# Performance work log

Measured on AMD Instinct MI355X. Metric: run time of the kernel, lower is better.

## Reference

```python
import jax, jax.numpy as jnp
import numpy as np

D_HIDDEN = 400
D_ANCHOR = 31
N_LAYER = 24
N_HEADS = 8
DIM_HEAD = 400
D_INNER = 800
D_STATE = 16
D_CONV = 4
DT_RANK = 25  # ceil(400/16)
PE_HIDDEN = 48
EPS = 1e-5


def _point_embed(x, w, b):
    # Fourier point embedding (3DShape2VecSet PointEmbed), dim-major freq layout.
    d = x.shape[-1]
    nf = PE_HIDDEN // (2 * d)
    freqs = (2.0 ** jnp.arange(nf, dtype=x.dtype)) * jnp.pi  # [nf]
    proj = (x[..., None] * freqs).reshape(*x.shape[:-1], d * nf)  # [b,n,d*nf]
    emb = jnp.concatenate([jnp.sin(proj), jnp.cos(proj), x], axis=-1)  # [b,n,48+d]
    return emb @ w.T + b


def _rmsnorm(x, w):
    return x * jax.lax.rsqrt(jnp.mean(x * x, axis=-1, keepdims=True) + EPS) * w


def _layernorm(x, w, b):
    mu = jnp.mean(x, axis=-1, keepdims=True)
    var = jnp.var(x, axis=-1, keepdims=True)
    return (x - mu) * jax.lax.rsqrt(var + EPS) * w + b


def _selective_scan(u, dt, A, Bm, Cm, Dp):
    # u, dt: [b,l,di]; A: [di,n]; Bm, Cm: [b,l,n]; Dp: [di]
    def step(h, inp):
        u_t, dt_t, B_t, C_t = inp  # [b,di],[b,di],[b,n],[b,n]
        h = jnp.exp(dt_t[..., None] * A) * h + (dt_t * u_t)[..., None] * B_t[:, None, :]
        return h, jnp.einsum('bdn,bn->bd', h, C_t)
    h0 = jnp.zeros((u.shape[0], u.shape[2], A.shape[1]), u.dtype)
    xs = (jnp.swapaxes(u, 0, 1), jnp.swapaxes(dt, 0, 1),
          jnp.swapaxes(Bm, 0, 1), jnp.swapaxes(Cm, 0, 1))
    _, ys = jax.lax.scan(step, h0, xs)
    return jnp.swapaxes(ys, 0, 1) + u * Dp


def _mamba_block(x, norm_w, in_w, conv_w, conv_b, xproj_w, dt_w, dt_b, A_log, Dp, out_w):
    b, L, _ = x.shape
    xn = _rmsnorm(x, norm_w)
    u, z = jnp.split(xn @ in_w.T, 2, axis=-1)  # each [b,L,di]
    # causal depthwise conv1d, kernel D_CONV, left pad D_CONV-1 (torch conv truncated to L)
    u_pad = jnp.pad(u, ((0, 0), (D_CONV - 1, 0), (0, 0)))
    conv = sum(u_pad[:, k:k + L, :] * conv_w[:, k] for k in range(D_CONV)) + conv_b
    u_c = jax.nn.silu(conv)
    dbc = u_c @ xproj_w.T  # [b,L,dt_rank+2n]
    dt, Bm, Cm = jnp.split(dbc, [DT_RANK, DT_RANK + D_STATE], axis=-1)
    dt = jax.nn.softplus(dt @ dt_w.T + dt_b)  # [b,L,di]
    y = _selective_scan(u_c, dt, -jnp.exp(A_log), Bm, Cm, Dp)
    return x + (y * jax.nn.silu(z)) @ out_w.T


def _forward(mash_params, qry, anchor_w, anchor_b, point_w, point_b,
             norm_w, in_w, conv_w, conv_b, xproj_w, dt_w, dt_b, A_log, Dp, out_w,
             ln_q_w, ln_q_b, ln_c_w, ln_c_b, to_q_w, to_kv_w, to_out_w, to_out_b,
             ff_ln_w, ff_ln_b, ff_w1, ff_b1, ff_w2, ff_b2, head_w, head_b):
    # anchor embed on first 6 dims, concat remaining 25 -> [b,na,400]
    anc = _point_embed(mash_params[:, :, :6], anchor_w, anchor_b)
    x = jnp.concatenate([anc, mash_params[:, :, 6:]], axis=-1)
    for i in range(N_LAYER):
        x = _mamba_block(x, norm_w[i], in_w[i], conv_w[i], conv_b[i], xproj_w[i],
                         dt_w[i], dt_b[i], A_log[i], Dp[i], out_w[i])
    q_emb = _point_embed(qry, point_w, point_b)  # [b,nq,400]
    # PreNorm cross-attention (query norm + context norm), no residual
    qn = _layernorm(q_emb, ln_q_w, ln_q_b)
    ctx = _layernorm(x, ln_c_w, ln_c_b)
    b, nq, _ = qn.shape
    na = ctx.shape[1]
    q = (qn @ to_q_w.T).reshape(b, nq, N_HEADS, DIM_HEAD)
    k, v = jnp.split(ctx @ to_kv_w.T, 2, axis=-1)
    k = k.reshape(b, na, N_HEADS, DIM_HEAD)
    v = v.reshape(b, na, N_HEADS, DIM_HEAD)
    sim = jnp.einsum('bihd,bjhd->bhij', q, k) * (DIM_HEAD ** -0.5)
    attn = jax.nn.softmax(sim, axis=-1)
    out = jnp.einsum('bhij,bjhd->bihd', attn, v).reshape(b, nq, N_HEADS * DIM_HEAD)
    latents = out @ to_out_w.T + to_out_b  # [b,nq,400]
    # PreNorm GEGLU FeedForward with residual
    h = _layernorm(latents, ff_ln_w, ff_ln_b) @ ff_w1.T + ff_b1  # [b,nq,3200]
    a, g = jnp.split(h, 2, axis=-1)
    h = (a * jax.nn.gelu(g)) @ ff_w2.T + ff_b2
    latents = latents + h
    occ = (latents @ head_w.T + head_b).squeeze(-1)  # [b,nq]
    return occ


def setup_inputs() -> dict:
    key = jax.random.key(0)
    ks = iter(jax.random.split(key, 48))
    def nrm(shape, scale=0.02):
        return jax.random.normal(next(ks), shape, dtype=jnp.float32) * scale
    B, NA, NQ = 4, 400, 4096
    INNER = N_HEADS * DIM_HEAD  # 3200
    dt_init = jax.random.uniform(next(ks), (N_LAYER, D_INNER), minval=1e-3, maxval=0.1)
    inp = {
        'mash_params': nrm((B, NA, D_ANCHOR), 1.0),
        'qry': jax.random.uniform(next(ks), (B, NQ, 3), minval=-1.0, maxval=1.0),
        'anchor_w': nrm((D_HIDDEN - D_ANCHOR + 6, PE_HIDDEN + 6)),
        'anchor_b': jnp.zeros((D_HIDDEN - D_ANCHOR + 6,), jnp.float32),
        'point_w': nrm((D_HIDDEN, PE_HIDDEN + 3)),
        'point_b': jnp.zeros((D_HIDDEN,), jnp.float32),
        'norm_w': jnp.ones((N_LAYER, D_HIDDEN), jnp.float32),
        'in_w': nrm((N_LAYER, 2 * D_INNER, D_HIDDEN)),
        'conv_w': nrm((N_LAYER, D_INNER, D_CONV), 0.2),
        'conv_b': jnp.zeros((N_LAYER, D_INNER), jnp.float32),
        'xproj_w': nrm((N_LAYER, DT_RANK + 2 * D_STATE, D_INNER)),
        'dt_w': nrm((N_LAYER, D_INNER, DT_RANK), 0.1),
        'dt_b': jnp.log(jnp.expm1(dt_init)),
        'A_log': jnp.log(jnp.broadcast_to(jnp.arange(1, D_STATE + 1, dtype=jnp.float32),
                                          (N_LAYER, D_INNER, D_STATE))),
        'Dp': jnp.ones((N_LAYER, D_INNER), jnp.float32),
        'out_w': nrm((N_LAYER, D_HIDDEN, D_INNER)),
        'ln_q_w': jnp.ones((D_HIDDEN,), jnp.float32), 'ln_q_b': jnp.zeros((D_HIDDEN,), jnp.float32),
        'ln_c_w': jnp.ones((D_HIDDEN,), jnp.float32), 'ln_c_b': jnp.zeros((D_HIDDEN,), jnp.float32),
        'to_q_w': nrm((INNER, D_HIDDEN)),
        'to_kv_w': nrm((2 * INNER, D_HIDDEN)),
        'to_out_w': nrm((D_HIDDEN, INNER)),
        'to_out_b': jnp.zeros((D_HIDDEN,), jnp.float32),
        'ff_ln_w': jnp.ones((D_HIDDEN,), jnp.float32), 'ff_ln_b': jnp.zeros((D_HIDDEN,), jnp.float32),
        'ff_w1': nrm((8 * D_HIDDEN, D_HIDDEN)),
        'ff_b1': jnp.zeros((8 * D_HIDDEN,), jnp.float32),
        'ff_w2': nrm((D_HIDDEN, 4 * D_HIDDEN)),
        'ff_b2': jnp.zeros((D_HIDDEN,), jnp.float32),
        'head_w': nrm((1, D_HIDDEN)),
        'head_b': jnp.zeros((1,), jnp.float32),
    }
    return inp


def reference(mash_params, qry, anchor_w, anchor_b, point_w, point_b,
              norm_w, in_w, conv_w, conv_b, xproj_w, dt_w, dt_b, A_log, Dp, out_w,
              ln_q_w, ln_q_b, ln_c_w, ln_c_b, to_q_w, to_kv_w, to_out_w, to_out_b,
              ff_ln_w, ff_ln_b, ff_w1, ff_b1, ff_w2, ff_b2, head_w, head_b):
    return _forward(mash_params, qry, anchor_w, anchor_b, point_w, point_b,
                    norm_w, in_w, conv_w, conv_b, xproj_w, dt_w, dt_b, A_log, Dp, out_w,
                    ln_q_w, ln_q_b, ln_c_w, ln_c_b, to_q_w, to_kv_w, to_out_w, to_out_b,
                    ff_ln_w, ff_ln_b, ff_w1, ff_b1, ff_w2, ff_b2, head_w, head_b)
```

## Files before the change

### kernel.cpp

```cpp
#include <hip/hip_runtime.h>


#define EPI_NONE 0
#define EPI_SOFTPLUS 1
#define EPI_RES 2
#define EPI_GEGLU 3

typedef short bf16x8 __attribute__((ext_vector_type(8)));
typedef float f32x4 __attribute__((ext_vector_type(4)));

static __device__ __forceinline__ float silu_f(float x) {
  return x / (1.f + __expf(-x));
}
static __device__ __forceinline__ float softplus_f(float x) {
  return fmaxf(x, 0.f) + log1pf(__expf(-fabsf(x)));
}
static __device__ __forceinline__ float gelu_f(float x) {
  const float c = 0.7978845608028654f;
  return 0.5f * x * (1.f + tanhf(c * (x + 0.044715f * x * x * x)));
}
static __device__ __forceinline__ unsigned short f2bf(float f) {
  union { float f; unsigned int u; } v; v.f = f;
  unsigned int r = v.u + 0x7FFFu + ((v.u >> 16) & 1u);
  return (unsigned short)(r >> 16);
}
static __device__ __forceinline__ float bf2f(unsigned short h) {
  union { unsigned int u; float f; } v; v.u = ((unsigned int)h) << 16;
  return v.f;
}

__global__ void cvt_w_kernel(const float* __restrict__ src, unsigned short* __restrict__ dst,
                             int Lr, int R, int C, int Rp, int Cp) {
  size_t i8 = ((size_t)blockIdx.x * 256 + threadIdx.x) * 8;
// ... 19 lines not shown
  size_t total = (size_t)HB * 416 * 416;
  if (i8 >= total) return;
  int c = (int)(i8 % 416);
  int n = (int)(i8 / 416);
  int head = n / 416, r = n % 416;
  const float* s = src + ((size_t)(head * 400 + r)) * 400 + c;
  bf16x8 o;
#pragma unroll
  for (int q = 0; q < 8; ++q) {
    float v = (r < 400 && (c + q) < 400) ? s[q] : 0.f;
    o[q] = (short)f2bf(v);
  }
  *reinterpret_cast<bf16x8*>(dst + i8) = o;
}

__global__ void cvt_colhead_k(const float* __restrict__ src, unsigned short* __restrict__ dst,
                              int HB) {
  size_t i8 = ((size_t)blockIdx.x * 256 + threadIdx.x) * 8;
  size_t total = (size_t)512 * HB * 416;
  if (i8 >= total) return;
  int cp = (int)(i8 % ((size_t)HB * 416));
  int r = (int)(i8 / ((size_t)HB * 416));
  int head = cp / 416, cc = cp % 416;
  bf16x8 o;
#pragma unroll
  for (int q = 0; q < 8; ++q) {
    int c = cc + q;
    float v = (r < 400 && c < 400) ? src[(size_t)r * (HB * 400) + head * 400 + c] : 0.f;
    o[q] = (short)f2bf(v);
  }
  *reinterpret_cast<bf16x8*>(dst + i8) = o;
}

template <int EPI, int OUTBF>
__global__ __launch_bounds__(256) void gemm_bf16_k(
    const unsigned short* __restrict__ A, int lda, long long zsA,
    const unsigned short* __restrict__ W, int ldw, long long zsW,
    const float* __restrict__ bias,
    const float* __restrict__ aux, int ldaux,
    void* __restrict__ Cout, int ldc, long long zsC,
    int M, int N, int K) {
  __shared__ unsigned short As[128 * 32];
  __shared__ unsigned short Bs[128 * 32];
  const int tid = threadIdx.x;
  const int lane = tid & 63;
  const int wid = tid >> 6;
  const int wr = wid >> 1, wc = wid & 1;
  const int m0 = blockIdx.y * 128, n0 = blockIdx.x * 128;
  const long long z = blockIdx.z;
  A += z * zsA;
  W += z * zsW;

  f32x4 acc[4][4];
#pragma unroll
  for (int i = 0; i < 4; ++i)
#pragma unroll
    for (int j = 0; j < 4; ++j) acc[i][j] = (f32x4){0.f, 0.f, 0.f, 0.f};

  const int i0 = tid;
  const int i1 = tid + 256;
  const unsigned short* gA0 = A + (size_t)(m0 + (i0 >> 2)) * lda + ((i0 & 3) << 3);
  const unsigned short* gA1 = A + (size_t)(m0 + (i1 >> 2)) * lda + ((i1 & 3) << 3);
  const unsigned short* gB0 = W + (size_t)(n0 + (i0 >> 2)) * ldw + ((i0 & 3) << 3);
  const unsigned short* gB1 = W + (size_t)(n0 + (i1 >> 2)) * ldw + ((i1 & 3) << 3);
  unsigned short* lA0 = &As[i0 * 8];
  unsigned short* lA1 = &As[i1 * 8];
  unsigned short* lB0 = &Bs[i0 * 8];
  unsigned short* lB1 = &Bs[i1 * 8];

  const int fr = lane & 15, fq = lane >> 4;
  const int arow = wr * 64 + fr;
  const int brow = wc * 64 + fr;

  for (int k0 = 0; k0 < K; k0 += 32) {
    __builtin_amdgcn_global_load_lds(
        (const __attribute__((address_space(1))) unsigned int*)(gA0 + k0),
        (__attribute__((address_space(3))) unsigned int*)lA0, 16, 0, 0);
    __builtin_amdgcn_global_load_lds(
        (const __attribute__((address_space(1))) unsigned int*)(gA1 + k0),
        (__attribute__((address_space(3))) unsigned int*)lA1, 16, 0, 0);
    __builtin_amdgcn_global_load_lds(
        (const __attribute__((address_space(1))) unsigned int*)(gB0 + k0),
        (__attribute__((address_space(3))) unsigned int*)lB0, 16, 0, 0);
    __builtin_amdgcn_global_load_lds(
        (const __attribute__((address_space(1))) unsigned int*)(gB1 + k0),
        (__attribute__((address_space(3))) unsigned int*)lB1, 16, 0, 0);
    __syncthreads();
    bf16x8 av[4], bv[4];
#pragma unroll
    for (int mi = 0; mi < 4; ++mi)
      av[mi] = *reinterpret_cast<const bf16x8*>(&As[(arow + mi * 16) * 32 + fq * 8]);
#pragma unroll
    for (int ni = 0; ni < 4; ++ni)
      bv[ni] = *reinterpret_cast<const bf16x8*>(&Bs[(brow + ni * 16) * 32 + fq * 8]);
#pragma unroll
    for (int mi = 0; mi < 4; ++mi)
#pragma unroll
      for (int ni = 0; ni < 4; ++ni)
        acc[mi][ni] =
            __builtin_amdgcn_mfma_f32_16x16x32_bf16(av[mi], bv[ni], acc[mi][ni], 0, 0, 0);
    __syncthreads();
  }

  float* Cf = (float*)Cout + z * zsC;
  unsigned short* Cb = (unsigned short*)Cout + z * zsC;
  const float* auxp = aux ? aux + z * zsC : aux;
#pragma unroll
  for (int mi = 0; mi < 4; ++mi) {
#pragma unroll
    for (int r = 0; r < 4; ++r) {
      int m = m0 + wr * 64 + mi * 16 + fq * 4 + r;
      if (m >= M) continue;
#pragma unroll
      for (int ni = 0; ni < 4; ++ni) {
        int n = n0 + wc * 64 + ni * 16 + fr;
        if (n >= N) continue;
        float v = acc[mi][ni][r];
        if (bias) v += bias[n];
        if (EPI == EPI_GEGLU) v = auxp[(size_t)m * ldaux + n] * gelu_f(v);
        else if (EPI == EPI_RES) v += auxp[(size_t)m * ldaux + n];
        if (OUTBF) Cb[(size_t)m * ldc + n] = f2bf(v);
        else Cf[(size_t)m * ldc + n] = v;
      }
    }
  }
}

template <int BM, int BN, int BK, int TM, int TN, int EPI>
__global__ __launch_bounds__(256) void gemm_k(
    const float* __restrict__ A, int lda,
    const float* __restrict__ W, int ldw,
    const float* __restrict__ bias,
    float* __restrict__ C, int ldc,
    int M, int N, int K) {
  __shared__ float As[BK][BM];
  __shared__ float Bs[BK][BN];
  const int tid = threadIdx.x;
  const int tx = tid % (BN / TN);
  const int ty = tid / (BN / TN);
  const int m0 = blockIdx.y * BM;
  const int n0 = blockIdx.x * BN;

  float acc[TM][TN];
#pragma unroll
  for (int i = 0; i < TM; ++i)
#pragma unroll
    for (int j = 0; j < TN; ++j) acc[i][j] = 0.f;

  const int a_row = (tid * 4) / BK;
  const int a_col = (tid * 4) % BK;

  for (int k0 = 0; k0 < K; k0 += BK) {
    {
      int gm = m0 + a_row, gk = k0 + a_col;
      float4 v = make_float4(0.f, 0.f, 0.f, 0.f);
      if (gm < M) {
        if (gk + 3 < K) {
          v = *reinterpret_cast<const float4*>(A + (size_t)gm * lda + gk);
        } else {
          float tmp[4];
#pragma unroll
          for (int q = 0; q < 4; ++q)
            tmp[q] = (gk + q < K) ? A[(size_t)gm * lda + gk + q] : 0.f;
          v = make_float4(tmp[0], tmp[1], tmp[2], tmp[3]);
        }
      }
      As[a_col + 0][a_row] = v.x;
      As[a_col + 1][a_row] = v.y;
      As[a_col + 2][a_row] = v.z;
      As[a_col + 3][a_row] = v.w;
    }
    {
      int gn = n0 + a_row, gk = k0 + a_col;
      float4 v = make_float4(0.f, 0.f, 0.f, 0.f);
      if (gn < N) {
        if (gk + 3 < K) {
          v = *reinterpret_cast<const float4*>(W + (size_t)gn * ldw + gk);
        } else {
          float tmp[4];
#pragma unroll
          for (int q = 0; q < 4; ++q)
            tmp[q] = (gk + q < K) ? W[(size_t)gn * ldw + gk + q] : 0.f;
          v = make_float4(tmp[0], tmp[1], tmp[2], tmp[3]);
        }
      }
      Bs[a_col + 0][a_row] = v.x;
      Bs[a_col + 1][a_row] = v.y;
      Bs[a_col + 2][a_row] = v.z;
      Bs[a_col + 3][a_row] = v.w;
    }
    __syncthreads();
#pragma unroll
    for (int kk = 0; kk < BK; ++kk) {
      float a[TM], bb[TN];
#pragma unroll
      for (int i = 0; i < TM; i += 4)
        *reinterpret_cast<float4*>(&a[i]) =
            *reinterpret_cast<const float4*>(&As[kk][ty * TM + i]);
#pragma unroll
      for (int j = 0; j < TN; j += 4)
        *reinterpret_cast<float4*>(&bb[j]) =
            *reinterpret_cast<const float4*>(&Bs[kk][tx * TN + j]);
#pragma unroll
      for (int i = 0; i < TM; ++i)
#pragma unroll
        for (int j = 0; j < TN; ++j) acc[i][j] = fmaf(a[i], bb[j], acc[i][j]);
    }
    __syncthreads();
  }

#pragma unroll
  for (int i = 0; i < TM; ++i) {
    int m = m0 + ty * TM + i;
    if (m >= M) continue;
#pragma unroll
    for (int j = 0; j < TN; ++j) {
      int n = n0 + tx * TN + j;
      if (n >= N) continue;
      float v = acc[i][j];
      if (bias) v += bias[n];
      if (EPI == EPI_SOFTPLUS) v = softplus_f(v);
      C[(size_t)m * ldc + n] = v;
    }
  }
}

__global__ void anchor_embed_kernel(const float* __restrict__ mash,
                                    float* __restrict__ aemb) {
  int row = blockIdx.x;
  int lane = threadIdx.x;
  if (lane >= 54) return;
  const float PI = 3.14159265358979323846f;
  float e;
  if (lane < 48) {
    int j = (lane < 24) ? lane : lane - 24;
    int d = j >> 2, f = j & 3;
    float v = mash[row * 31 + d] * (PI * (float)(1 << f));
    e = (lane < 24) ? sinf(v) : cosf(v);
  } else {
    e = mash[row * 31 + (lane - 48)];
  }
  aemb[row * 54 + lane] = e;
}

__global__ void point_embed_q_kernel(const float* __restrict__ qry,
                                     unsigned short* __restrict__ qep) {
  int row = blockIdx.x;
  int lane = threadIdx.x;
  const float PI = 3.14159265358979323846f;
  float e = 0.f;
  if (lane < 48) {
    int j = (lane < 24) ? lane : lane - 24;
    int d = j >> 3, f = j & 7;
    float v = qry[row * 3 + d] * (PI * (float)(1 << f));
    e = (lane < 24) ? sinf(v) : cosf(v);
  } else if (lane < 51) {
    e = qry[row * 3 + (lane - 48)];
  }
  qep[(size_t)row * 64 + lane] = f2bf(e);
}

__global__ void copy_tail_kernel(const float* __restrict__ mash,
                                 float* __restrict__ x) {
  int idx = blockIdx.x * 256 + threadIdx.x;
  if (idx >= 1600 * 25) return;
  int row = idx / 25, j = idx % 25;
  x[row * 400 + 375 + j] = mash[row * 31 + 6 + j];
}

__global__ void rmsnorm_bf16_kernel(const float* __restrict__ x,
                                    const float* __restrict__ w,
                                    unsigned short* __restrict__ out) {
  int row = blockIdx.x;
  int lane = threadIdx.x;
  float ss = 0.f;
  float vals[7];
  int nv = 0;
  for (int c = lane; c < 400; c += 64) {
    float v = x[(size_t)row * 400 + c];
    vals[nv++] = v;
    ss += v * v;
  }
#pragma unroll
  for (int off = 1; off < 64; off <<= 1) ss += __shfl_xor(ss, off);
  float r = rsqrtf(ss * (1.f / 400.f) + 1e-5f);
  nv = 0;
  for (int c = lane; c < 416; c += 64) {
    unsigned short o = 0;
    if (c < 400) o = f2bf(vals[nv++] * r * w[c]);
    out[(size_t)row * 416 + c] = o;
  }
}

__global__ void layernorm_bf16_kernel(const float* __restrict__ x,
                                      const float* __restrict__ w,
                                      const float* __restrict__ b,
                                      unsigned short* __restrict__ out) {
  int row = blockIdx.x;
  int lane = threadIdx.x;
  float s = 0.f, s2 = 0.f;
  float vals[7];
  int nv = 0;
  for (int c = lane; c < 400; c += 64) {
    float v = x[(size_t)row * 400 + c];
    vals[nv++] = v;
    s += v;
    s2 += v * v;
  }
#pragma unroll
  for (int off = 1; off < 64; off <<= 1) {
    s += __shfl_xor(s, off);
    s2 += __shfl_xor(s2, off);
  }
  float mu = s * (1.f / 400.f);
  float var = s2 * (1.f / 400.f) - mu * mu;
  float r = rsqrtf(var + 1e-5f);
  nv = 0;
  for (int c = lane; c < 416; c += 64) {
    unsigned short o = 0;
    if (c < 400) o = f2bf((vals[nv++] - mu) * r * w[c] + b[c]);
    out[(size_t)row * 416 + c] = o;
  }
}

__global__ void conv_silu_kernel(const float* __restrict__ uz,
                                 const float* __restrict__ cw,
                                 const float* __restrict__ cb,
                                 unsigned short* __restrict__ ucb,
                                 float* __restrict__ uc32) {
  int idx = (blockIdx.x * 256 + threadIdx.x) * 4;
  if (idx >= 1600 * 800) return;
  int c = idx % 800;
  int row = idx / 800;
  int l = row % 400;
  int b = row / 400;
  const float* ub = uz + (size_t)b * 400 * 1600 + c;
  float4 acc = *reinterpret_cast<const float4*>(cb + c);
  float wk[4][4];
#pragma unroll
  for (int i = 0; i < 4; ++i) {
    float4 t = *reinterpret_cast<const float4*>(cw + (size_t)(c + i) * 4);
    wk[i][0] = t.x; wk[i][1] = t.y; wk[i][2] = t.z; wk[i][3] = t.w;
  }
#pragma unroll
  for (int k = 0; k < 4; ++k) {
    int ls = l - 3 + k;
    if (ls < 0) continue;
    float4 u = *reinterpret_cast<const float4*>(ub + (size_t)ls * 1600);
    acc.x = fmaf(u.x, wk[0][k], acc.x);
    acc.y = fmaf(u.y, wk[1][k], acc.y);
    acc.z = fmaf(u.z, wk[2][k], acc.z);
    acc.w = fmaf(u.w, wk[3][k], acc.w);
  }
  float4 v = make_float4(silu_f(acc.x), silu_f(acc.y), silu_f(acc.z), silu_f(acc.w));
  *reinterpret_cast<float4*>(uc32 + idx) = v;
  union { unsigned short s[4]; uint2 u; } o;
  o.s[0] = f2bf(v.x); o.s[1] = f2bf(v.y); o.s[2] = f2bf(v.z); o.s[3] = f2bf(v.w);
  *reinterpret_cast<uint2*>(ucb + idx) = o.u;
}

__global__ void scan_kernel(const float* __restrict__ uc,
                            const float* __restrict__ dt,
                            const float* __restrict__ dbc,
                            const float* __restrict__ uz,
                            const float* __restrict__ A_log,
                            const float* __restrict__ Dp,
                            unsigned short* __restrict__ gb) {
  int t = blockIdx.x * 256 + threadIdx.x;
  if (t >= 12800) return;
  int g = t & 3;
  int bd = t >> 2;
  int b = bd / 800;
  int d = bd - b * 800;
  float A0 = -__expf(A_log[d * 16 + g * 4 + 0]);
  float A1 = -__expf(A_log[d * 16 + g * 4 + 1]);
  float A2 = -__expf(A_log[d * 16 + g * 4 + 2]);
  float A3 = -__expf(A_log[d * 16 + g * 4 + 3]);
  float Dpd = Dp[d];
  float h0 = 0.f, h1 = 0.f, h2 = 0.f, h3 = 0.f;
  const int off = 25 + g * 4;
  for (int l0 = 0; l0 < 400; l0 += 4) {
    float dtv[4], uv[4], zv[4], Bv[4][4], Cv[4][4];
#pragma unroll
    for (int q = 0; q < 4; ++q) {
      size_t base = (size_t)(b * 400 + l0 + q);
      dtv[q] = dt[base * 800 + d];
      uv[q] = uc[base * 800 + d];
      zv[q] = uz[base * 1600 + 800 + d];
      const float* bc = dbc + base * 64 + off;
#pragma unroll
      for (int s = 0; s < 4; ++s) {
        Bv[q][s] = bc[s];
        Cv[q][s] = bc[16 + s];
      }
    }
#pragma unroll
    for (int q = 0; q < 4; ++q) {
      float du = dtv[q] * uv[q];
      h0 = __expf(dtv[q] * A0) * h0 + du * Bv[q][0];
      h1 = __expf(dtv[q] * A1) * h1 + du * Bv[q][1];
      h2 = __expf(dtv[q] * A2) * h2 + du * Bv[q][2];
      h3 = __expf(dtv[q] * A3) * h3 + du * Bv[q][3];
      float yv = h0 * Cv[q][0] + h1 * Cv[q][1] + h2 * Cv[q][2] + h3 * Cv[q][3];
      yv += __shfl_xor(yv, 1);
      yv += __shfl_xor(yv, 2);
      if (g == 0) {
        size_t base = (size_t)(b * 400 + l0 + q);
        gb[base * 800 + d] = f2bf((yv + uv[q] * Dpd) * silu_f(zv[q]));
      }
    }
  }
}

__global__ void softmax_k(float* S) {
  int row = blockIdx.x * 4 + (threadIdx.x >> 6);
  int lane = threadIdx.x & 63;
  float* sr = S + (size_t)row * 416;
  float v[7];
  float m = -1e30f;
#pragma unroll
  for (int i = 0; i < 7; ++i) {
    int c = lane + i * 64;
    v[i] = (c < 400) ? sr[c] : -1e30f;
    m = fmaxf(m, v[i]);
  }
#pragma unroll
  for (int off = 1; off < 64; off <<= 1) m = fmaxf(m, __shfl_xor(m, off));
  float sum = 0.f;
#pragma unroll
  for (int i = 0; i < 7; ++i) {
    int c = lane + i * 64;
    float p = (c < 400) ? __expf(0.05f * (v[i] - m)) : 0.f;
    v[i] = p;
    sum += p;
  }
#pragma unroll
  for (int off = 1; off < 64; off <<= 1) sum += __shfl_xor(sum, off);
  float inv = 1.f / sum;
  unsigned short* pr = (unsigned short*)sr;
#pragma unroll
  for (int i = 0; i < 7; ++i) {
    int c = lane + i * 64;
    if (c < 400) pr[c] = f2bf(v[i] * inv);
// ... 112 lines not shown

  if (ws_size < TOTAL * sizeof(float)) return;

  float* ws = (float*)d_ws;
  float* X   = ws + XOFF;
  float* LAT = ws + LATO;
  unsigned short* pWI  = (unsigned short*)(ws + WI);
  unsigned short* pWX  = (unsigned short*)(ws + WX);
  unsigned short* pWO  = (unsigned short*)(ws + WO);
  unsigned short* pWK  = (unsigned short*)(ws + WK);
  unsigned short* pWV  = (unsigned short*)(ws + WV);
  unsigned short* pWP  = (unsigned short*)(ws + WP);
  unsigned short* pWQ  = (unsigned short*)(ws + WQ);
  unsigned short* pWTO = (unsigned short*)(ws + WTO);
  unsigned short* pWF1 = (unsigned short*)(ws + WF1);
  unsigned short* pWF2 = (unsigned short*)(ws + WF2);

  cvt_w_kernel<<<cvtblocks(24LL*1664*416), 256, 0, stream>>>(in_w,   pWI, 24, 1600, 400, 1664, 416);
  cvt_w_kernel<<<cvtblocks(24LL*128*800),  256, 0, stream>>>(xproj_w,pWX, 24, 57,   800, 128,  800);
  cvt_w_kernel<<<cvtblocks(24LL*512*800),  256, 0, stream>>>(out_w,  pWO, 24, 400,  800, 512,  800);
  cvt_headrow_k<<<cvtblocks(8LL*416*416),  256, 0, stream>>>(to_kv_w, pWK, 8);
  cvt_headrow_k<<<cvtblocks(8LL*416*416),  256, 0, stream>>>(to_kv_w + 3200LL*400, pWV, 8);
  cvt_w_kernel<<<cvtblocks(512LL*64),      256, 0, stream>>>(point_w, pWP, 1, 400, 51, 512, 64);
  cvt_headrow_k<<<cvtblocks(8LL*416*416),  256, 0, stream>>>(to_q_w, pWQ, 8);
  cvt_colhead_k<<<cvtblocks(512LL*8*416),  256, 0, stream>>>(to_out_w, pWTO, 8);
  cvt_w_kernel<<<cvtblocks(3264LL*416),    256, 0, stream>>>(ff_w1, pWF1, 1, 3200, 400, 3264, 416);
  cvt_w_kernel<<<cvtblocks(512LL*1600),    256, 0, stream>>>(ff_w2, pWF2, 1, 400, 1600, 512, 1600);

  anchor_embed_kernel<<<1600, 64, 0, stream>>>(mash, ws + AEMB);
  gemm_k<64, 64, 16, 4, 4, EPI_NONE><<<dim3(6, 25), 256, 0, stream>>>(
      ws + AEMB, 54, anchor_w, 54, anchor_b, X, 400, 1600, 375, 54);
  copy_tail_kernel<<<cdiv(1600 * 25, 256), 256, 0, stream>>>(mash, X);

  for (int L = 0; L < 24; ++L) {
    rmsnorm_bf16_kernel<<<1600, 64, 0, stream>>>(X, norm_w + (size_t)L * 400,
                                                 (unsigned short*)(ws + XNB));
    gemm_bf16_k<EPI_NONE, 0><<<dim3(13, 13), 256, 0, stream>>>(
        (unsigned short*)(ws + XNB), 416, 0, pWI + (size_t)L * 1664 * 416, 416, 0,
        nullptr, nullptr, 0, ws + UZ, 1600, 0, 1600, 1600, 416);
    conv_silu_kernel<<<1250, 256, 0, stream>>>(
        ws + UZ, conv_w + (size_t)L * 3200, conv_b + (size_t)L * 800,
        (unsigned short*)(ws + UCB), ws + UC32);
    gemm_bf16_k<EPI_NONE, 0><<<dim3(1, 13), 256, 0, stream>>>(
        (unsigned short*)(ws + UCB), 800, 0, pWX + (size_t)L * 128 * 800, 800, 0,
        nullptr, nullptr, 0, ws + DBC, 64, 0, 1600, 57, 800);
    gemm_k<64, 64, 16, 4, 4, EPI_SOFTPLUS><<<dim3(13, 25), 256, 0, stream>>>(
        ws + DBC, 64, dt_w + (size_t)L * 800 * 25, 25, dt_b + (size_t)L * 800,
        ws + DTO, 800, 1600, 800, 25);
    scan_kernel<<<50, 256, 0, stream>>>(ws + UC32, ws + DTO, ws + DBC, ws + UZ,
                                        A_log + (size_t)L * 12800,
                                        Dp + (size_t)L * 800,
                                        (unsigned short*)(ws + GB));
    gemm_bf16_k<EPI_RES, 0><<<dim3(4, 13), 256, 0, stream>>>(
        (unsigned short*)(ws + GB), 800, 0, pWO + (size_t)L * 512 * 800, 800, 0,
        nullptr, X, 400, X, 400, 0, 1600, 400, 800);
  }

  unsigned short* CTX = (unsigned short*)(ws + OB);
  layernorm_bf16_kernel<<<1600, 64, 0, stream>>>(X, ln_c_w, ln_c_b, CTX);
  gemm_bf16_k<EPI_NONE, 1><<<dim3(26, 13), 256, 0, stream>>>(
      CTX, 416, 0, pWK, 416, 0, nullptr, nullptr, 0,
      (unsigned short*)(ws + KB), 3328, 0, 1600, 3328, 416);
  gemm_bf16_k<EPI_NONE, 1><<<dim3(26, 13), 256, 0, stream>>>(
      CTX, 416, 0, pWV, 416, 0, nullptr, nullptr, 0,
      (unsigned short*)(ws + VB), 3328, 0, 1600, 3328, 416);
  vt_repack_k<<<dim3(13, 8, 32), 256, 0, stream>>>(
      (unsigned short*)(ws + VB), (unsigned short*)(ws + VT8));

  point_embed_q_kernel<<<16384, 64, 0, stream>>>(qry, (unsigned short*)(ws + QEP));
  gemm_bf16_k<EPI_NONE, 0><<<dim3(4, 128), 256, 0, stream>>>(
      (unsigned short*)(ws + QEP), 64, 0, pWP, 64, 0, point_b, nullptr, 0,
      ws + QEMB, 400, 0, 16384, 400, 64);
  layernorm_bf16_kernel<<<16384, 64, 0, stream>>>(ws + QEMB, ln_q_w, ln_q_b,
                                                  (unsigned short*)(ws + QN));

  for (int b = 0; b < 4; ++b) {
    gemm_bf16_k<EPI_NONE, 1><<<dim3(4, 32, 8), 256, 0, stream>>>(
        (unsigned short*)(ws + QN) + (size_t)b * 4096 * 416, 416, 0,
        pWQ, 416, 416LL * 416, nullptr, nullptr, 0,
        (unsigned short*)(ws + QH8), 416, 4096LL * 416, 4096, 416, 416);
    for (int half = 0; half < 2; ++half) {
      const unsigned short* Aq =
          (unsigned short*)(ws + QH8) + (size_t)half * 2048 * 416;
      gemm_bf16_k<EPI_NONE, 0><<<dim3(4, 16, 8), 256, 0, stream>>>(
          Aq, 416, 4096LL * 416,
          (unsigned short*)(ws + KB) + (size_t)b * 400 * 3328, 3328, 416LL,
          nullptr, nullptr, 0, ws + SOFF, 416, 2048LL * 416, 2048, 400, 416);
      softmax_k<<<4096, 256, 0, stream>>>(ws + SOFF);
// ... 31 lines not shown
```

Before: 8.044 ms.

## Fuse 24 Mamba layers into one cooperative persistent kernel with grid syncs

Replaces the per-layer sequence of seven kernel launches (rmsnorm, in-proj GEMM, conv+silu, x-proj GEMM, dt-proj, scan, out-proj GEMM) with a single cooperative kernel of 256 blocks that loops over the 24 layers and uses grid.sync between stages. This is meant to remove about 168 launch overheads and the gaps between dependent small kernels. The dt projection is also changed from a tiled fp32 GEMM to a direct per-element dot product, and the old per-layer launches are kept as a fallback if the cooperative launch fails. The cost is that many blocks sit idle in the narrow stages (the scan uses 50 blocks, the x-proj GEMM 13), plus the latency of each grid barrier.

Result: slower. 12.63 ms (+57.1%).

```diff
diff --git a/kernel.cpp b/kernel.cpp
--- a/kernel.cpp
+++ b/kernel.cpp
@@ -1,4 +1,6 @@
 #include <hip/hip_runtime.h>
+#include <hip/hip_cooperative_groups.h>
+namespace cg = cooperative_groups;
 
 
 #define EPI_NONE 0
@@ -84,24 +86,17 @@
   *reinterpret_cast<bf16x8*>(dst + i8) = o;
 }
 
-template <int EPI, int OUTBF>
-__global__ __launch_bounds__(256) void gemm_bf16_k(
-    const unsigned short* __restrict__ A, int lda, long long zsA,
-    const unsigned short* __restrict__ W, int ldw, long long zsW,
-    const float* __restrict__ bias,
-    const float* __restrict__ aux, int ldaux,
-    void* __restrict__ Cout, int ldc, long long zsC,
-    int M, int N, int K) {
-  __shared__ unsigned short As[128 * 32];
-  __shared__ unsigned short Bs[128 * 32];
+template <int RES>
+static __device__ void tile_gemm_f32(const unsigned short* __restrict__ A, int lda,
+                                     const unsigned short* __restrict__ W, int ldw,
+                                     float* __restrict__ C, int ldc,
+                                     const float* __restrict__ aux, int ldaux,
+                                     int m0, int n0, int M, int N, int K,
+                                     unsigned short* As, unsigned short* Bs) {
   const int tid = threadIdx.x;
   const int lane = tid & 63;
   const int wid = tid >> 6;
   const int wr = wid >> 1, wc = wid & 1;
-  const int m0 = blockIdx.y * 128, n0 = blockIdx.x * 128;
-  const long long z = blockIdx.z;
-  A += z * zsA;
-  W += z * zsW;
 
   f32x4 acc[4][4];
 #pragma unroll
@@ -154,9 +149,6 @@
     __syncthreads();
   }
 
-  float* Cf = (float*)Cout + z * zsC;
-  unsigned short* Cb = (unsigned short*)Cout + z * zsC;
-  const float* auxp = aux ? aux + z * zsC : aux;
 #pragma unroll
   for (int mi = 0; mi < 4; ++mi) {
 #pragma unroll
@@ -168,156 +160,182 @@
         int n = n0 + wc * 64 + ni * 16 + fr;
         if (n >= N) continue;
         float v = acc[mi][ni][r];
-        if (bias) v += bias[n];
-        if (EPI == EPI_GEGLU) v = auxp[(size_t)m * ldaux + n] * gelu_f(v);
-        else if (EPI == EPI_RES) v += auxp[(size_t)m * ldaux + n];
-        if (OUTBF) Cb[(size_t)m * ldc + n] = f2bf(v);
-        else Cf[(size_t)m * ldc + n] = v;
+        if (RES) v += aux[(size_t)m * ldaux + n];
+        C[(size_t)m * ldc + n] = v;
       }
     }
   }
 }
 
-template <int BM, int BN, int BK, int TM, int TN, int EPI>
-__global__ __launch_bounds__(256) void gemm_k(
-    const float* __restrict__ A, int lda,
-    const float* __restrict__ W, int ldw,
-    const float* __restrict__ bias,
-    float* __restrict__ C, int ldc,
-    int M, int N, int K) {
-  __shared__ float As[BK][BM];
-  __shared__ float Bs[BK][BN];
+struct MambaArgs {
+  const float* norm_w;
+  const float* conv_w;
+  const float* conv_b;
+  const float* dt_w;
+  const float* dt_b;
+  const float* A_log;
+  const float* Dp;
+  const unsigned short* pWI;
+  const unsigned short* pWX;
+  const unsigned short* pWO;
+  float* X;
+  unsigned short* XNB;
+  float* UZ;
+  unsigned short* UCB;
+  float* UC32;
+  float* DBC;
+  float* DTO;
+  unsigned short* GB;
+};
+
+__global__ __launch_bounds__(256) void mamba_coop_k(MambaArgs a) {
+  __shared__ unsigned short As[128 * 32];
+  __shared__ unsigned short Bs[128 * 32];
+  cg::grid_group grid = cg::this_grid();
+  const int bid = blockIdx.x;
   const int tid = threadIdx.x;
-  const int tx = tid % (BN / TN);
-  const int ty = tid / (BN / TN);
-  const int m0 = blockIdx.y * BM;
-  const int n0 = blockIdx.x * BN;
-
-  float acc[TM][TN];
-#pragma unroll
-  for (int i = 0; i < TM; ++i)
-#pragma unroll
-    for (int j = 0; j < TN; ++j) acc[i][j] = 0.f;
-
-  const int a_row = (tid * 4) / BK;
-  const int a_col = (tid * 4) % BK;
-
-  for (int k0 = 0; k0 < K; k0 += BK) {
+  const int w = tid >> 6, lane = tid & 63;
+
+  for (int L = 0; L < 24; ++L) {
+    const unsigned short* WI = a.pWI + (size_t)L * 1664 * 416;
+    const unsigned short* WX = a.pWX + (size_t)L * 128 * 800;
+    const unsigned short* WO = a.pWO + (size_t)L * 512 * 800;
+    const float* nw = a.norm_w + (size_t)L * 400;
+
+    for (int r = bid * 4 + w; r < 1600; r += 1024) {
+      float ss = 0.f;
+      float vals[7];
+      int nv = 0;
+      for (int c = lane; c < 400; c += 64) {
+        float v = a.X[(size_t)r * 400 + c];
+        vals[nv++] = v;
+        ss += v * v;
+      }
+#pragma unroll
+      for (int off = 1; off < 64; off <<= 1) ss += __shfl_xor(ss, off);
+      float rr = rsqrtf(ss * (1.f / 400.f) + 1e-5f);
+      nv = 0;
+      for (int c = lane; c < 416; c += 64) {
+        unsigned short o = 0;
+        if (c < 400) o = f2bf(vals[nv++] * rr * nw[c]);
+        a.XNB[(size_t)r * 416 + c] = o;
+      }
+    }
+    grid.sync();
+
+    if (bid < 169)
+      tile_gemm_f32<0>(a.XNB, 416, WI, 416, a.UZ, 1600, nullptr, 0,
+                       (bid / 13) * 128, (bid % 13) * 128, 1600, 1600, 416, As, Bs);
+    grid.sync();
+
     {
-      int gm = m0 + a_row, gk = k0 + a_col;
-      float4 v = make_float4(0.f, 0.f, 0.f, 0.f);
-      if (gm < M) {
-        if (gk + 3 < K) {
-          v = *reinterpret_cast<const float4*>(A + (size_t)gm * lda + gk);
-        } else {
-          float tmp[4];
-#pragma unroll
-          for (int q = 0; q < 4; ++q)
-            tmp[q] = (gk + q < K) ? A[(size_t)gm * lda + gk + q] : 0.f;
-          v = make_float4(tmp[0], tmp[1], tmp[2], tmp[3]);
+      const float* cw = a.conv_w + (size_t)L * 3200;
+      const float* cb = a.conv_b + (size_t)L * 800;
+      for (int idx = (bid * 256 + tid) * 4; idx < 1600 * 800; idx += 262144) {
+        int c = idx % 800;
+        int row = idx / 800;
+        int l = row % 400;
+        int b = row / 400;
+        const float* ub = a.UZ + (size_t)b * 400 * 1600 + c;
+        float4 acc4 = *reinterpret_cast<const float4*>(cb + c);
+        float wk[4][4];
+#pragma unroll
+        for (int i = 0; i < 4; ++i) {
+          float4 t = *reinterpret_cast<const float4*>(cw + (size_t)(c + i) * 4);
+          wk[i][0] = t.x; wk[i][1] = t.y; wk[i][2] = t.z; wk[i][3] = t.w;
+        }
+#pragma unroll
+        for (int k = 0; k < 4; ++k) {
+          int ls = l - 3 + k;
+          if (ls < 0) continue;
+          float4 u = *reinterpret_cast<const float4*>(ub + (size_t)ls * 1600);
+          acc4.x = fmaf(u.x, wk[0][k], acc4.x);
+          acc4.y = fmaf(u.y, wk[1][k], acc4.y);
+          acc4.z = fmaf(u.z, wk[2][k], acc4.z);
+          acc4.w = fmaf(u.w, wk[3][k], acc4.w);
+        }
+        float4 v = make_float4(silu_f(acc4.x), silu_f(acc4.y), silu_f(acc4.z), silu_f(acc4.w));
+        *reinterpret_cast<float4*>(a.UC32 + idx) = v;
+        union { unsigned short s[4]; uint2 u; } o;
+        o.s[0] = f2bf(v.x); o.s[1] = f2bf(v.y); o.s[2] = f2bf(v.z); o.s[3] = f2bf(v.w);
+        *reinterpret_cast<uint2*>(a.UCB + idx) = o.u;
+      }
+    }
+    grid.sync();
+
+    if (bid < 13)
+      tile_gemm_f32<0>(a.UCB, 800, WX, 800, a.DBC, 64, nullptr, 0,
+                       bid * 128, 0, 1600, 57, 800, As, Bs);
+    grid.sync();
+
+    {
+      const float* dtwL = a.dt_w + (size_t)L * 800 * 25;
+      const float* dtbL = a.dt_b + (size_t)L * 800;
+      for (int t = bid * 256 + tid; t < 1600 * 800; t += 65536) {
+        int r = t / 800, c = t - r * 800;
+        const float* dr = a.DBC + (size_t)r * 64;
+        const float* wr2 = dtwL + (size_t)c * 25;
+        float s = dtbL[c];
+#pragma unroll
+        for (int k = 0; k < 25; ++k) s = fmaf(dr[k], wr2[k], s);
+        a.DTO[t] = softplus_f(s);
+      }
+    }
+    grid.sync();
+
+    if (bid < 50) {
+      int t = bid * 256 + tid;
+      int g = t & 3;
+      int bd = t >> 2;
+      int b = bd / 800;
+      int d = bd - b * 800;
+      const float* AlogL = a.A_log + (size_t)L * 12800;
+      float A0 = -__expf(AlogL[d * 16 + g * 4 + 0]);
+      float A1 = -__expf(AlogL[d * 16 + g * 4 + 1]);
+      float A2 = -__expf(AlogL[d * 16 + g * 4 + 2]);
+      float A3 = -__expf(AlogL[d * 16 + g * 4 + 3]);
+      float Dpd = a.Dp[(size_t)L * 800 + d];
+      float h0 = 0.f, h1 = 0.f, h2 = 0.f, h3 = 0.f;
+      const int off = 25 + g * 4;
+      for (int l0 = 0; l0 < 400; l0 += 4) {
+        float dtv[4], uv[4], zv[4], Bv[4][4], Cv[4][4];
+#pragma unroll
+        for (int q = 0; q < 4; ++q) {
+          size_t base = (size_t)(b * 400 + l0 + q);
+          dtv[q] = a.DTO[base * 800 + d];
+          uv[q] = a.UC32[base * 800 + d];
+          zv[q] = a.UZ[base * 1600 + 800 + d];
+          const float* bc = a.DBC + base * 64 + off;
+#pragma unroll
+          for (int s = 0; s < 4; ++s) {
+            Bv[q][s] = bc[s];
+            Cv[q][s] = bc[16 + s];
+          }
+        }
+#pragma unroll
+        for (int q = 0; q < 4; ++q) {
+          float du = dtv[q] * uv[q];
+          h0 = __expf(dtv[q] * A0) * h0 + du * Bv[q][0];
+          h1 = __expf(dtv[q] * A1) * h1 + du * Bv[q][1];
+          h2 = __expf(dtv[q] * A2) * h2 + du * Bv[q][2];
+          h3 = __expf(dtv[q] * A3) * h3 + du * Bv[q][3];
+          float yv = h0 * Cv[q][0] + h1 * Cv[q][1] + h2 * Cv[q][2] + h3 * Cv[q][3];
+          yv += __shfl_xor(yv, 1);
+          yv += __shfl_xor(yv, 2);
+          if (g == 0) {
+            size_t base = (size_t)(b * 400 + l0 + q);
+            a.GB[base * 800 + d] = f2bf((yv + uv[q] * Dpd) * silu_f(zv[q]));
+          }
         }
       }
-      As[a_col + 0][a_row] = v.x;
-      As[a_col + 1][a_row] = v.y;
-      As[a_col + 2][a_row] = v.z;
-      As[a_col + 3][a_row] = v.w;
-    }
-    {
-      int gn = n0 + a_row, gk = k0 + a_col;
-      float4 v = make_float4(0.f, 0.f, 0.f, 0.f);
-      if (gn < N) {
-        if (gk + 3 < K) {
-          v = *reinterpret_cast<const float4*>(W + (size_t)gn * ldw + gk);
-        } else {
-          float tmp[4];
-#pragma unroll
-          for (int q = 0; q < 4; ++q)
-            tmp[q] = (gk + q < K) ? W[(size_t)gn * ldw + gk + q] : 0.f;
-          v = make_float4(tmp[0], tmp[1], tmp[2], tmp[3]);
-        }
-      }
-      Bs[a_col + 0][a_row] = v.x;
-      Bs[a_col + 1][a_row] = v.y;
-      Bs[a_col + 2][a_row] = v.z;
-      Bs[a_col + 3][a_row] = v.w;
-    }
-    __syncthreads();
-#pragma unroll
-    for (int kk = 0; kk < BK; ++kk) {
-      float a[TM], bb[TN];
-#pragma unroll
-      for (int i = 0; i < TM; i += 4)
-        *reinterpret_cast<float4*>(&a[i]) =
-            *reinterpret_cast<const float4*>(&As[kk][ty * TM + i]);
-#pragma unroll
-      for (int j = 0; j < TN; j += 4)
-        *reinterpret_cast<float4*>(&bb[j]) =
-            *reinterpret_cast<const float4*>(&Bs[kk][tx * TN + j]);
-#pragma unroll
-      for (int i = 0; i < TM; ++i)
-#pragma unroll
-        for (int j = 0; j < TN; ++j) acc[i][j] = fmaf(a[i], bb[j], acc[i][j]);
-    }
-    __syncthreads();
-  }
-
-#pragma unroll
-  for (int i = 0; i < TM; ++i) {
-    int m = m0 + ty * TM + i;
-    if (m >= M) continue;
-#pragma unroll
-    for (int j = 0; j < TN; ++j) {
-      int n = n0 + tx * TN + j;
-      if (n >= N) continue;
-      float v = acc[i][j];
-      if (bias) v += bias[n];
-      if (EPI == EPI_SOFTPLUS) v = softplus_f(v);
-      C[(size_t)m * ldc + n] = v;
-    }
-  }
-}
-
-__global__ void anchor_embed_kernel(const float* __restrict__ mash,
-                                    float* __restrict__ aemb) {
-  int row = blockIdx.x;
-  int lane = threadIdx.x;
-  if (lane >= 54) return;
-  const float PI = 3.14159265358979323846f;
-  float e;
-  if (lane < 48) {
-    int j = (lane < 24) ? lane : lane - 24;
-    int d = j >> 2, f = j & 3;
-    float v = mash[row * 31 + d] * (PI * (float)(1 << f));
-    e = (lane < 24) ? sinf(v) : cosf(v);
-  } else {
-    e = mash[row * 31 + (lane - 48)];
-  }
-  aemb[row * 54 + lane] = e;
-}
-
-__global__ void point_embed_q_kernel(const float* __restrict__ qry,
-                                     unsigned short* __restrict__ qep) {
-  int row = blockIdx.x;
-  int lane = threadIdx.x;
-  const float PI = 3.14159265358979323846f;
-  float e = 0.f;
-  if (lane < 48) {
-    int j = (lane < 24) ? lane : lane - 24;
-    int d = j >> 3, f = j & 7;
-    float v = qry[row * 3 + d] * (PI * (float)(1 << f));
-    e = (lane < 24) ? sinf(v) : cosf(v);
-  } else if (lane < 51) {
-    e = qry[row * 3 + (lane - 48)];
-  }
-  qep[(size_t)row * 64 + lane] = f2bf(e);
-}
-
-__global__ void copy_tail_kernel(const float* __restrict__ mash,
-                                 float* __restrict__ x) {
-  int idx = blockIdx.x * 256 + threadIdx.x;
-  if (idx >= 1600 * 25) return;
-  int row = idx / 25, j = idx % 25;
-  x[row * 400 + 375 + j] = mash[row * 31 + 6 + j];
+    }
+    grid.sync();
+
+    if (bid < 52)
+      tile_gemm_f32<1>(a.GB, 800, WO, 800, a.X, 400, a.X, 400,
+                       (bid % 13) * 128, (bid / 13) * 128, 1600, 400, 800, As, Bs);
+    grid.sync();
+  }
 }
 
 __global__ void rmsnorm_bf16_kernel(const float* __restrict__ x,
@@ -340,37 +358,6 @@
   for (int c = lane; c < 416; c += 64) {
     unsigned short o = 0;
     if (c < 400) o = f2bf(vals[nv++] * r * w[c]);
-    out[(size_t)row * 416 + c] = o;
-  }
-}
-
-__global__ void layernorm_bf16_kernel(const float* __restrict__ x,
-                                      const float* __restrict__ w,
-                                      const float* __restrict__ b,
-                                      unsigned short* __restrict__ out) {
-  int row = blockIdx.x;
-  int lane = threadIdx.x;
-  float s = 0.f, s2 = 0.f;
-  float vals[7];
-  int nv = 0;
-  for (int c = lane; c < 400; c += 64) {
-    float v = x[(size_t)row * 400 + c];
-    vals[nv++] = v;
-    s += v;
-    s2 += v * v;
-  }
-#pragma unroll
-  for (int off = 1; off < 64; off <<= 1) {
-    s += __shfl_xor(s, off);
-    s2 += __shfl_xor(s2, off);
-  }
-  float mu = s * (1.f / 400.f);
-  float var = s2 * (1.f / 400.f) - mu * mu;
-  float r = rsqrtf(var + 1e-5f);
-  nv = 0;
-  for (int c = lane; c < 416; c += 64) {
-    unsigned short o = 0;
-    if (c < 400) o = f2bf((vals[nv++] - mu) * r * w[c] + b[c]);
     out[(size_t)row * 416 + c] = o;
   }
 }
@@ -409,6 +396,21 @@
   union { unsigned short s[4]; uint2 u; } o;
   o.s[0] = f2bf(v.x); o.s[1] = f2bf(v.y); o.s[2] = f2bf(v.z); o.s[3] = f2bf(v.w);
   *reinterpret_cast<uint2*>(ucb + idx) = o.u;
+}
+
+__global__ void dtproj_kernel(const float* __restrict__ dbc,
+                              const float* __restrict__ dtw,
+                              const float* __restrict__ dtb,
+                              float* __restrict__ out) {
+  int t = blockIdx.x * 256 + threadIdx.x;
+  if (t >= 1600 * 800) return;
+  int r = t / 800, c = t - r * 800;
+  const float* dr = dbc + (size_t)r * 64;
+  const float* wr = dtw + (size_t)c * 25;
+  float s = dtb[c];
+#pragma unroll
+  for (int k = 0; k < 25; ++k) s = fmaf(dr[k], wr[k], s);
+  out[t] = softplus_f(s);
 }
 
 __global__ void scan_kernel(const float* __restrict__ uc,
@@ -461,6 +463,273 @@
         gb[base * 800 + d] = f2bf((yv + uv[q] * Dpd) * silu_f(zv[q]));
       }
     }
+  }
+}
+
+template <int EPI, int OUTBF>
+__global__ __launch_bounds__(256) void gemm_bf16_k(
+    const unsigned short* __restrict__ A, int lda, long long zsA,
+    const unsigned short* __restrict__ W, int ldw, long long zsW,
+    const float* __restrict__ bias,
+    const float* __restrict__ aux, int ldaux,
+    void* __restrict__ Cout, int ldc, long long zsC,
+    int M, int N, int K) {
+  __shared__ unsigned short As[128 * 32];
+  __shared__ unsigned short Bs[128 * 32];
+  const int tid = threadIdx.x;
+  const int lane = tid & 63;
+  const int wid = tid >> 6;
+  const int wr = wid >> 1, wc = wid & 1;
+  const int m0 = blockIdx.y * 128, n0 = blockIdx.x * 128;
+  const long long z = blockIdx.z;
+  A += z * zsA;
+  W += z * zsW;
+
+  f32x4 acc[4][4];
+#pragma unroll
+  for (int i = 0; i < 4; ++i)
+#pragma unroll
+    for (int j = 0; j < 4; ++j) acc[i][j] = (f32x4){0.f, 0.f, 0.f, 0.f};
+
+  const int i0 = tid;
+  const int i1 = tid + 256;
+  const unsigned short* gA0 = A + (size_t)(m0 + (i0 >> 2)) * lda + ((i0 & 3) << 3);
+  const unsigned short* gA1 = A + (size_t)(m0 + (i1 >> 2)) * lda + ((i1 & 3) << 3);
+  const unsigned short* gB0 = W + (size_t)(n0 + (i0 >> 2)) * ldw + ((i0 & 3) << 3);
+  const unsigned short* gB1 = W + (size_t)(n0 + (i1 >> 2)) * ldw + ((i1 & 3) << 3);
+  unsigned short* lA0 = &As[i0 * 8];
+  unsigned short* lA1 = &As[i1 * 8];
+  unsigned short* lB0 = &Bs[i0 * 8];
+  unsigned short* lB1 = &Bs[i1 * 8];
+
+  const int fr = lane & 15, fq = lane >> 4;
+  const int arow = wr * 64 + fr;
+  const int brow = wc * 64 + fr;
+
+  for (int k0 = 0; k0 < K; k0 += 32) {
+    __builtin_amdgcn_global_load_lds(
+        (const __attribute__((address_space(1))) unsigned int*)(gA0 + k0),
+        (__attribute__((address_space(3))) unsigned int*)lA0, 16, 0, 0);
+    __builtin_amdgcn_global_load_lds(
+        (const __attribute__((address_space(1))) unsigned int*)(gA1 + k0),
+        (__attribute__((address_space(3))) unsigned int*)lA1, 16, 0, 0);
+    __builtin_amdgcn_global_load_lds(
+        (const __attribute__((address_space(1))) unsigned int*)(gB0 + k0),
+        (__attribute__((address_space(3))) unsigned int*)lB0, 16, 0, 0);
+    __builtin_amdgcn_global_load_lds(
+        (const __attribute__((address_space(1))) unsigned int*)(gB1 + k0),
+        (__attribute__((address_space(3))) unsigned int*)lB1, 16, 0, 0);
+    __syncthreads();
+    bf16x8 av[4], bv[4];
+#pragma unroll
+    for (int mi = 0; mi < 4; ++mi)
+      av[mi] = *reinterpret_cast<const bf16x8*>(&As[(arow + mi * 16) * 32 + fq * 8]);
+#pragma unroll
+    for (int ni = 0; ni < 4; ++ni)
+      bv[ni] = *reinterpret_cast<const bf16x8*>(&Bs[(brow + ni * 16) * 32 + fq * 8]);
+#pragma unroll
+    for (int mi = 0; mi < 4; ++mi)
+#pragma unroll
+      for (int ni = 0; ni < 4; ++ni)
+        acc[mi][ni] =
+            __builtin_amdgcn_mfma_f32_16x16x32_bf16(av[mi], bv[ni], acc[mi][ni], 0, 0, 0);
+    __syncthreads();
+  }
+
+  float* Cf = (float*)Cout + z * zsC;
+  unsigned short* Cb = (unsigned short*)Cout + z * zsC;
+  const float* auxp = aux ? aux + z * zsC : aux;
+#pragma unroll
+  for (int mi = 0; mi < 4; ++mi) {
+#pragma unroll
+    for (int r = 0; r < 4; ++r) {
+      int m = m0 + wr * 64 + mi * 16 + fq * 4 + r;
+      if (m >= M) continue;
+#pragma unroll
+      for (int ni = 0; ni < 4; ++ni) {
+        int n = n0 + wc * 64 + ni * 16 + fr;
+        if (n >= N) continue;
+        float v = acc[mi][ni][r];
+        if (bias) v += bias[n];
+        if (EPI == EPI_GEGLU) v = auxp[(size_t)m * ldaux + n] * gelu_f(v);
+        else if (EPI == EPI_RES) v += auxp[(size_t)m * ldaux + n];
+        if (OUTBF) Cb[(size_t)m * ldc + n] = f2bf(v);
+        else Cf[(size_t)m * ldc + n] = v;
+      }
+    }
+  }
+}
+
+template <int BM, int BN, int BK, int TM, int TN, int EPI>
+__global__ __launch_bounds__(256) void gemm_k(
+    const float* __restrict__ A, int lda,
+    const float* __restrict__ W, int ldw,
+    const float* __restrict__ bias,
+    float* __restrict__ C, int ldc,
+    int M, int N, int K) {
+  __shared__ float As[BK][BM];
+  __shared__ float Bs[BK][BN];
+  const int tid = threadIdx.x;
+  const int tx = tid % (BN / TN);
+  const int ty = tid / (BN / TN);
+  const int m0 = blockIdx.y * BM;
+  const int n0 = blockIdx.x * BN;
+
+  float acc[TM][TN];
+#pragma unroll
+  for (int i = 0; i < TM; ++i)
+#pragma unroll
+    for (int j = 0; j < TN; ++j) acc[i][j] = 0.f;
+
+  const int a_row = (tid * 4) / BK;
+  const int a_col = (tid * 4) % BK;
+
+  for (int k0 = 0; k0 < K; k0 += BK) {
+    {
+      int gm = m0 + a_row, gk = k0 + a_col;
+      float4 v = make_float4(0.f, 0.f, 0.f, 0.f);
+      if (gm < M) {
+        if (gk + 3 < K) {
+          v = *reinterpret_cast<const float4*>(A + (size_t)gm * lda + gk);
+        } else {
+          float tmp[4];
+#pragma unroll
+          for (int q = 0; q < 4; ++q)
+            tmp[q] = (gk + q < K) ? A[(size_t)gm * lda + gk + q] : 0.f;
+          v = make_float4(tmp[0], tmp[1], tmp[2], tmp[3]);
+        }
+      }
+      As[a_col + 0][a_row] = v.x;
+      As[a_col + 1][a_row] = v.y;
+      As[a_col + 2][a_row] = v.z;
+      As[a_col + 3][a_row] = v.w;
+    }
+    {
+      int gn = n0 + a_row, gk = k0 + a_col;
+      float4 v = make_float4(0.f, 0.f, 0.f, 0.f);
+      if (gn < N) {
+        if (gk + 3 < K) {
+          v = *reinterpret_cast<const float4*>(W + (size_t)gn * ldw + gk);
+        } else {
+          float tmp[4];
+#pragma unroll
+          for (int q = 0; q < 4; ++q)
+            tmp[q] = (gk + q < K) ? W[(size_t)gn * ldw + gk + q] : 0.f;
+          v = make_float4(tmp[0], tmp[1], tmp[2], tmp[3]);
+        }
+      }
+      Bs[a_col + 0][a_row] = v.x;
+      Bs[a_col + 1][a_row] = v.y;
+      Bs[a_col + 2][a_row] = v.z;
+      Bs[a_col + 3][a_row] = v.w;
+    }
+    __syncthreads();
+#pragma unroll
+    for (int kk = 0; kk < BK; ++kk) {
+      float a[TM], bb[TN];
+#pragma unroll
+      for (int i = 0; i < TM; i += 4)
+        *reinterpret_cast<float4*>(&a[i]) =
+            *reinterpret_cast<const float4*>(&As[kk][ty * TM + i]);
+#pragma unroll
+      for (int j = 0; j < TN; j += 4)
+        *reinterpret_cast<float4*>(&bb[j]) =
+            *reinterpret_cast<const float4*>(&Bs[kk][tx * TN + j]);
+#pragma unroll
+      for (int i = 0; i < TM; ++i)
+#pragma unroll
+        for (int j = 0; j < TN; ++j) acc[i][j] = fmaf(a[i], bb[j], acc[i][j]);
+    }
+    __syncthreads();
+  }
+
+#pragma unroll
+  for (int i = 0; i < TM; ++i) {
+    int m = m0 + ty * TM + i;
+    if (m >= M) continue;
+#pragma unroll
+    for (int j = 0; j < TN; ++j) {
+      int n = n0 + tx * TN + j;
+      if (n >= N) continue;
+      float v = acc[i][j];
+      if (bias) v += bias[n];
+      if (EPI == EPI_SOFTPLUS) v = softplus_f(v);
+      C[(size_t)m * ldc + n] = v;
+    }
+  }
+}
+
+__global__ void anchor_embed_kernel(const float* __restrict__ mash,
+                                    float* __restrict__ aemb) {
+  int row = blockIdx.x;
+  int lane = threadIdx.x;
+  if (lane >= 54) return;
+  const float PI = 3.14159265358979323846f;
+  float e;
+  if (lane < 48) {
+    int j = (lane < 24) ? lane : lane - 24;
+    int d = j >> 2, f = j & 3;
+    float v = mash[row * 31 + d] * (PI * (float)(1 << f));
+    e = (lane < 24) ? sinf(v) : cosf(v);
+  } else {
+    e = mash[row * 31 + (lane - 48)];
+  }
+  aemb[row * 54 + lane] = e;
+}
+
+__global__ void point_embed_q_kernel(const float* __restrict__ qry,
+                                     unsigned short* __restrict__ qep) {
+  int row = blockIdx.x;
+  int lane = threadIdx.x;
+  const float PI = 3.14159265358979323846f;
+  float e = 0.f;
+  if (lane < 48) {
+    int j = (lane < 24) ? lane : lane - 24;
+    int d = j >> 3, f = j & 7;
+    float v = qry[row * 3 + d] * (PI * (float)(1 << f));
+    e = (lane < 24) ? sinf(v) : cosf(v);
+  } else if (lane < 51) {
+    e = qry[row * 3 + (lane - 48)];
+  }
+  qep[(size_t)row * 64 + lane] = f2bf(e);
+}
+
+__global__ void copy_tail_kernel(const float* __restrict__ mash,
+                                 float* __restrict__ x) {
+  int idx = blockIdx.x * 256 + threadIdx.x;
+  if (idx >= 1600 * 25) return;
+  int row = idx / 25, j = idx % 25;
+  x[row * 400 + 375 + j] = mash[row * 31 + 6 + j];
+}
+
+__global__ void layernorm_bf16_kernel(const float* __restrict__ x,
+                                      const float* __restrict__ w,
+                                      const float* __restrict__ b,
+                                      unsigned short* __restrict__ out) {
+  int row = blockIdx.x;
+  int lane = threadIdx.x;
+  float s = 0.f, s2 = 0.f;
+  float vals[7];
+  int nv = 0;
+  for (int c = lane; c < 400; c += 64) {
+    float v = x[(size_t)row * 400 + c];
+    vals[nv++] = v;
+    s += v;
+    s2 += v * v;
+  }
+#pragma unroll
+  for (int off = 1; off < 64; off <<= 1) {
+    s += __shfl_xor(s, off);
+    s2 += __shfl_xor(s2, off);
+  }
+  float mu = s * (1.f / 400.f);
+  float var = s2 * (1.f / 400.f) - mu * mu;
+  float r = rsqrtf(var + 1e-5f);
+  nv = 0;
+  for (int c = lane; c < 416; c += 64) {
+    unsigned short o = 0;
+    if (c < 400) o = f2bf((vals[nv++] - mu) * r * w[c] + b[c]);
+    out[(size_t)row * 416 + c] = o;
   }
 }
 
@@ -639,28 +908,44 @@
       ws + AEMB, 54, anchor_w, 54, anchor_b, X, 400, 1600, 375, 54);
   copy_tail_kernel<<<cdiv(1600 * 25, 256), 256, 0, stream>>>(mash, X);
 
-  for (int L = 0; L < 24; ++L) {
-    rmsnorm_bf16_kernel<<<1600, 64, 0, stream>>>(X, norm_w + (size_t)L * 400,
-                                                 (unsigned short*)(ws + XNB));
-    gemm_bf16_k<EPI_NONE, 0><<<dim3(13, 13), 256, 0, stream>>>(
-        (unsigned short*)(ws + XNB), 416, 0, pWI + (size_t)L * 1664 * 416, 416, 0,
-        nullptr, nullptr, 0, ws + UZ, 1600, 0, 1600, 1600, 416);
-    conv_silu_kernel<<<1250, 256, 0, stream>>>(
-        ws + UZ, conv_w + (size_t)L * 3200, conv_b + (size_t)L * 800,
-        (unsigned short*)(ws + UCB), ws + UC32);
-    gemm_bf16_k<EPI_NONE, 0><<<dim3(1, 13), 256, 0, stream>>>(
-        (unsigned short*)(ws + UCB), 800, 0, pWX + (size_t)L * 128 * 800, 800, 0,
-        nullptr, nullptr, 0, ws + DBC, 64, 0, 1600, 57, 800);
-    gemm_k<64, 64, 16, 4, 4, EPI_SOFTPLUS><<<dim3(13, 25), 256, 0, stream>>>(
-        ws + DBC, 64, dt_w + (size_t)L * 800 * 25, 25, dt_b + (size_t)L * 800,
-        ws + DTO, 800, 1600, 800, 25);
-    scan_kernel<<<50, 256, 0, stream>>>(ws + UC32, ws + DTO, ws + DBC, ws + UZ,
-                                        A_log + (size_t)L * 12800,
-                                        Dp + (size_t)L * 800,
-                                        (unsigned short*)(ws + GB));
-    gemm_bf16_k<EPI_RES, 0><<<dim3(4, 13), 256, 0, stream>>>(
-        (unsigned short*)(ws + GB), 800, 0, pWO + (size_t)L * 512 * 800, 800, 0,
-        nullptr, X, 400, X, 400, 0, 1600, 400, 800);
+  MambaArgs ma;
+  ma.norm_w = norm_w; ma.conv_w = conv_w; ma.conv_b = conv_b;
+  ma.dt_w = dt_w; ma.dt_b = dt_b; ma.A_log = A_log; ma.Dp = Dp;
+  ma.pWI = pWI; ma.pWX = pWX; ma.pWO = pWO;
+  ma.X = X;
+  ma.XNB = (unsigned short*)(ws + XNB);
+  ma.UZ = ws + UZ;
+  ma.UCB = (unsigned short*)(ws + UCB);
+  ma.UC32 = ws + UC32;
+  ma.DBC = ws + DBC;
+  ma.DTO = ws + DTO;
+  ma.GB = (unsigned short*)(ws + GB);
+  void* kp[] = {(void*)&ma};
+  hipError_t cerr = hipLaunchCooperativeKernel((const void*)mamba_coop_k, dim3(256),
+                                               dim3(256), kp, 0, stream);
+  if (cerr != hipSuccess) {
+    for (int L = 0; L < 24; ++L) {
+      rmsnorm_bf16_kernel<<<1600, 64, 0, stream>>>(X, norm_w + (size_t)L * 400,
+                                                   (unsigned short*)(ws + XNB));
+      gemm_bf16_k<EPI_NONE, 0><<<dim3(13, 13), 256, 0, stream>>>(
+          (unsigned short*)(ws + XNB), 416, 0, pWI + (size_t)L * 1664 * 416, 416, 0,
+          nullptr, nullptr, 0, ws + UZ, 1600, 0, 1600, 1600, 416);
+      conv_silu_kernel<<<1250, 256, 0, stream>>>(
+          ws + UZ, conv_w + (size_t)L * 3200, conv_b + (size_t)L * 800,
+          (unsigned short*)(ws + UCB), ws + UC32);
+      gemm_bf16_k<EPI_NONE, 0><<<dim3(1, 13), 256, 0, stream>>>(
+          (unsigned short*)(ws + UCB), 800, 0, pWX + (size_t)L * 128 * 800, 800, 0,
+          nullptr, nullptr, 0, ws + DBC, 64, 0, 1600, 57, 800);
+      dtproj_kernel<<<cdiv(1600 * 800, 256), 256, 0, stream>>>(
+          ws + DBC, dt_w + (size_t)L * 800 * 25, dt_b + (size_t)L * 800, ws + DTO);
+      scan_kernel<<<50, 256, 0, stream>>>(ws + UC32, ws + DTO, ws + DBC, ws + UZ,
+                                          A_log + (size_t)L * 12800,
+                                          Dp + (size_t)L * 800,
+                                          (unsigned short*)(ws + GB));
+      gemm_bf16_k<EPI_RES, 0><<<dim3(4, 13), 256, 0, stream>>>(
+          (unsigned short*)(ws + GB), 800, 0, pWO + (size_t)L * 512 * 800, 800, 0,
+          nullptr, X, 400, X, 400, 0, 1600, 400, 800);
+    }
   }
 
   unsigned short* CTX = (unsigned short*)(ws + OB);
```
